# Optimization experiments

Hardware: AMD Instinct MI355X
Metric: run time of the kernel (lower is better)

Reference implementation:

```python
import jax, jax.numpy as jnp
import numpy as np

N = 24000; E = 384000; NT = 3; IN = 128; HID = 32; ED = 64; NE = 5; FFN = 64; C = 16
HEADS = (8, 8, 1); ALPHA = 0.05; DAL = 2


def _lrelu(x, s):
    return jnp.where(x >= 0, x, s * x)


def _elu(x):
    return jnp.where(x > 0, x, jnp.expm1(x))


def _ln(x, g, b, eps=1e-5):
    m = x.mean(-1, keepdims=True)
    v = ((x - m) ** 2).mean(-1, keepdims=True)
    return (x - m) / jnp.sqrt(v + eps) * g + b


def _l2n(x, eps=1e-12):
    return x / jnp.maximum(jnp.linalg.norm(x, axis=1, keepdims=True), eps)


def _ta(h, src, dst, e_feat, edge_emb, W, We, al, ar, ae, bias, res_W, res_attn, act):
    # SimpleHGN-style heterogeneous graph attention layer (TALayer)
    Hh = al.shape[0]
    feat = (h @ W).reshape(N, Hh, HID)                       # [N,H,D]
    ee = (edge_emb[e_feat] @ We).reshape(E, Hh, ED)          # [E,H,ED]
    el = (feat * al).sum(-1)                                 # [N,H]
    er = (feat * ar).sum(-1)                                 # [N,H]
    lg = _lrelu(el[src] + er[dst] + (ee * ae).sum(-1), 0.2)  # [E,H]
    m = jax.ops.segment_max(lg, dst, num_segments=N)         # edge softmax over dst
    a = jnp.exp(lg - m[dst])
    a = a / jax.ops.segment_sum(a, dst, num_segments=N)[dst]
    if res_attn is not None:
        a = a * (1.0 - ALPHA) + res_attn * ALPHA             # residual attention carry-over
    rst = jax.ops.segment_sum(a[:, :, None] * feat[src], dst, num_segments=N)
    if res_W is not None:
        rst = rst + (h @ res_W).reshape(N, Hh, HID)
    rst = rst + bias
    if act:
        rst = _elu(rst)
    return rst, jax.lax.stop_gradient(a)


def forward(feats, fc_W, fc_b, ntype_emb, W_ntype,
            ta0_edge_emb, ta0_W, ta0_We, ta0_al, ta0_ar, ta0_ae, ta0_bias,
            ta1_edge_emb, ta1_W, ta1_We, ta1_al, ta1_ar, ta1_ae, ta1_bias, ta1_res_W,
            ta2_edge_emb, ta2_W, ta2_We, ta2_al, ta2_ar, ta2_ae, ta2_bias, ta2_res_W,
            da_ln1_g, da_ln1_b, da_Wq, da_bq, da_Wk, da_bk, da_Wv, da_bv, da_Wo, da_bo,
            da_ln2_g, da_ln2_b, da_W1, da_b1, da_W2, da_b2, final_W, logits_W,
            e_feat, node_type, src, dst):
    # per-node-type input projection + leaky_relu(0.01), concat over types -> [N,HID]
    h = _lrelu(jnp.einsum('tni,tio->tno', feats, fc_W) + fc_b[:, None, :], 0.01).reshape(N, HID)
    ntype_feat = (ntype_emb @ W_ntype)[node_type]            # [N,HID]
    h = h * ntype_feat
    h0, a0 = _ta(h, src, dst, e_feat, ta0_edge_emb, ta0_W, ta0_We, ta0_al, ta0_ar, ta0_ae, ta0_bias, None, None, True)
    h = h0.reshape(N, -1)
    h1, _ = _ta(h, src, dst, e_feat, ta1_edge_emb, ta1_W, ta1_We, ta1_al, ta1_ar, ta1_ae, ta1_bias, ta1_res_W, a0, True)
    h = h1.reshape(N, -1)
    hf, _ = _ta(h, src, dst, e_feat, ta2_edge_emb, ta2_W, ta2_We, ta2_al, ta2_ar, ta2_ae, ta2_bias, ta2_res_W, None, False)
    h_feat = hf.reshape(N, HID)
    # dim-wise transformer (DALayer stack): tokens = HID dims, channel = 1
    x = (h_feat * ntype_feat)[:, :, None]                    # [N,HID,1]
    for l in range(DAL):
        y = _ln(x, da_ln1_g[l], da_ln1_b[l])
        q = y @ da_Wq[l] + da_bq[l]
        k = y @ da_Wk[l] + da_bk[l]
        v = y @ da_Wv[l] + da_bv[l]
        att = jax.nn.softmax(jnp.einsum('nqd,nkd->nqk', q, k), axis=-1)  # scale=att_size**-0.5=1
        x = x + (jnp.einsum('nqk,nkd->nqd', att, v) @ da_Wo[l] + da_bo[l])
        y = _ln(x, da_ln2_g[l], da_ln2_b[l])
        x = x + (jax.nn.gelu(y @ da_W1[l] + da_b1[l], approximate=False) @ da_W2[l] + da_b2[l])
    h_dim = _l2n(x[:, :, 0])
    h_final = jnp.concatenate([_l2n(h_feat), h_dim], axis=1) @ final_W
    logits = jax.nn.relu(h_final) @ logits_W
    return logits / jnp.maximum(jnp.linalg.norm(logits, axis=1, keepdims=True), 1e-12)


def setup_inputs():
    key = jax.random.key(0)
    ks = iter(jax.random.split(key, 96))
    def rn(shape, s=0.1):
        return jax.random.normal(next(ks), shape, jnp.float32) * s
    inp = {}
    inp["feats"] = jax.random.normal(next(ks), (NT, N // NT, IN), jnp.float32)
    inp["e_feat"] = jax.random.randint(next(ks), (E,), 0, NE)
    inp["node_type"] = jax.random.randint(next(ks), (N,), 0, NT)
    inp["src"] = jax.random.randint(next(ks), (E,), 0, N)
    inp["dst"] = jax.random.randint(next(ks), (E,), 0, N)
    inp["fc_W"] = rn((NT, IN, HID)); inp["fc_b"] = rn((NT, HID))
    inp["ntype_emb"] = rn((NT, HID)); inp["W_ntype"] = rn((HID, HID))
    ins = (HID, HID * HEADS[0], HID * HEADS[1])
    for l in range(3):
        Hh = HEADS[l]; di = ins[l]; p = "ta%d_" % l
        inp[p + "edge_emb"] = rn((NE, ED))
        inp[p + "W"] = rn((di, Hh * HID))
        inp[p + "We"] = rn((ED, Hh * ED))
        inp[p + "al"] = rn((Hh, HID)); inp[p + "ar"] = rn((Hh, HID)); inp[p + "ae"] = rn((Hh, ED))
        inp[p + "bias"] = jnp.zeros((Hh, HID), jnp.float32)
        if l > 0:
            inp[p + "res_W"] = rn((di, Hh * HID))
    inp["da_ln1_g"] = jnp.ones((DAL, 1), jnp.float32); inp["da_ln1_b"] = jnp.zeros((DAL, 1), jnp.float32)
    inp["da_Wq"] = rn((DAL, 1, 1)); inp["da_bq"] = jnp.zeros((DAL, 1), jnp.float32)
    inp["da_Wk"] = rn((DAL, 1, 1)); inp["da_bk"] = jnp.zeros((DAL, 1), jnp.float32)
    inp["da_Wv"] = rn((DAL, 1, 1)); inp["da_bv"] = jnp.zeros((DAL, 1), jnp.float32)
    inp["da_Wo"] = rn((DAL, 1, 1)); inp["da_bo"] = jnp.zeros((DAL, 1), jnp.float32)
    inp["da_ln2_g"] = jnp.ones((DAL, 1), jnp.float32); inp["da_ln2_b"] = jnp.zeros((DAL, 1), jnp.float32)
    inp["da_W1"] = rn((DAL, 1, FFN)); inp["da_b1"] = jnp.zeros((DAL, FFN), jnp.float32)
    inp["da_W2"] = rn((DAL, FFN, 1)); inp["da_b2"] = jnp.zeros((DAL, 1), jnp.float32)
    inp["final_W"] = rn((2 * HID, HID))
    inp["logits_W"] = rn((HID, C))
    return inp


def reference(feats, fc_W, fc_b, ntype_emb, W_ntype,
              ta0_edge_emb, ta0_W, ta0_We, ta0_al, ta0_ar, ta0_ae, ta0_bias,
              ta1_edge_emb, ta1_W, ta1_We, ta1_al, ta1_ar, ta1_ae, ta1_bias, ta1_res_W,
              ta2_edge_emb, ta2_W, ta2_We, ta2_al, ta2_ar, ta2_ae, ta2_bias, ta2_res_W,
              da_ln1_g, da_ln1_b, da_Wq, da_bq, da_Wk, da_bk, da_Wv, da_bv, da_Wo, da_bo,
              da_ln2_g, da_ln2_b, da_W1, da_b1, da_W2, da_b2, final_W, logits_W,
              e_feat, node_type, src, dst):
    return forward(feats, fc_W, fc_b, ntype_emb, W_ntype,
                   ta0_edge_emb, ta0_W, ta0_We, ta0_al, ta0_ar, ta0_ae, ta0_bias,
                   ta1_edge_emb, ta1_W, ta1_We, ta1_al, ta1_ar, ta1_ae, ta1_bias, ta1_res_W,
                   ta2_edge_emb, ta2_W, ta2_We, ta2_al, ta2_ar, ta2_ae, ta2_bias, ta2_res_W,
                   da_ln1_g, da_ln1_b, da_Wq, da_bq, da_Wk, da_bk, da_Wv, da_bv, da_Wo, da_bo,
                   da_ln2_g, da_ln2_b, da_W1, da_b1, da_W2, da_b2, final_W, logits_W,
                   e_feat, node_type, src, dst)
```

## Files before the change

### kernel.cpp

```cpp
#include <hip/hip_runtime.h>
#include <math.h>

constexpr int kN = 24000;
constexpr int kE = 384000;
constexpr float kAlpha = 0.05f;

typedef unsigned int   u32;
typedef unsigned short u16;
typedef __attribute__((ext_vector_type(8))) short short8;
typedef __attribute__((ext_vector_type(4))) float float4v;

__device__ __forceinline__ float bf2f(u16 x) { return __uint_as_float(((u32)x) << 16); }
__device__ __forceinline__ u16 f2bf(float f) {
  u32 u = __float_as_uint(f);
  return (u16)((u + 0x7fffu + ((u >> 16) & 1u)) >> 16);
}
__device__ __forceinline__ void bfrow32(const u16* __restrict__ p, float* f) {
  const uint4* q = (const uint4*)p;
  #pragma unroll
  for (int i = 0; i < 4; ++i) {
    uint4 w = q[i];
    f[i*8+0] = bf2f((u16)(w.x & 0xffff)); f[i*8+1] = bf2f((u16)(w.x >> 16));
    f[i*8+2] = bf2f((u16)(w.y & 0xffff)); f[i*8+3] = bf2f((u16)(w.y >> 16));
    f[i*8+4] = bf2f((u16)(w.z & 0xffff)); f[i*8+5] = bf2f((u16)(w.z >> 16));
    f[i*8+6] = bf2f((u16)(w.w & 0xffff)); f[i*8+7] = bf2f((u16)(w.w >> 16));
  }
}

__global__ void __launch_bounds__(256) zero_ints_kernel(int* __restrict__ p, int n) {
  int i = blockIdx.x * 256 + threadIdx.x;
  if (i < n) p[i] = 0;
}

__global__ void __launch_bounds__(256) count_kernel(const int* __restrict__ dst,
                                                    int* __restrict__ counts) {
  int e = blockIdx.x * 256 + threadIdx.x;
  if (e < kE) atomicAdd(&counts[dst[e]], 1);
}

__global__ void __launch_bounds__(1024) scan_kernel(const int* __restrict__ counts,
                                                    int* __restrict__ row_start) {
  __shared__ int wsum[16];
  __shared__ int carry_s;
  int tid = threadIdx.x, lane = tid & 63, wid = tid >> 6;
  if (tid == 0) { carry_s = 0; row_start[0] = 0; }
  __syncthreads();
  for (int base = 0; base < kN; base += 1024) {
    int x = (base + tid < kN) ? counts[base + tid] : 0;
    #pragma unroll
    for (int off = 1; off < 64; off <<= 1) {
      int y = __shfl_up(x, off);
      if (lane >= off) x += y;
    }
    if (lane == 63) wsum[wid] = x;
    __syncthreads();
    if (tid < 16) {
      int wv = wsum[tid];
      #pragma unroll
      for (int off = 1; off < 16; off <<= 1) {
        int y = __shfl_up(wv, off);
        if (tid >= off) wv += y;
      }
      wsum[tid] = wv;
    }
    __syncthreads();
    int incl = x + carry_s + (wid > 0 ? wsum[wid - 1] : 0);
    if (base + tid < kN) row_start[base + tid + 1] = incl;
    __syncthreads();
    if (tid == 1023) carry_s = incl;
    __syncthreads();
  }
}

__global__ void __launch_bounds__(256) scatter_kernel(const int* __restrict__ dst,
                                                      const int* __restrict__ row_start,
                                                      int* __restrict__ cursor,
                                                      int* __restrict__ edge_ids) {
  int e = blockIdx.x * 256 + threadIdx.x;
  if (e < kE) {
    int n = dst[e];
    int pos = row_start[n] + atomicAdd(&cursor[n], 1);
    edge_ids[pos] = e;
  }
}

__global__ void __launch_bounds__(256) prepack_kernel(
    const float* __restrict__ W0, const float* __restrict__ al0, const float* __restrict__ ar0,
    const float* __restrict__ W1, const float* __restrict__ al1, const float* __restrict__ ar1,
    const float* __restrict__ rW1,
    const float* __restrict__ W2, const float* __restrict__ al2, const float* __restrict__ ar2,
    const float* __restrict__ rW2,
    u16* __restrict__ WT0, u16* __restrict__ WT1, u16* __restrict__ WT2,
    const float* __restrict__ ntype_emb, const float* __restrict__ W_ntype,
    const float* __restrict__ emb0, const float* __restrict__ We0, const float* __restrict__ ae0,
    const float* __restrict__ emb1, const float* __restrict__ We1, const float* __restrict__ ae1,
    const float* __restrict__ emb2, const float* __restrict__ We2, const float* __restrict__ ae2,
    const float* __restrict__ ln1_b, const float* __restrict__ Wv, const float* __restrict__ bv,
    const float* __restrict__ Wo, const float* __restrict__ bo,
    const float* __restrict__ ln2_b, const float* __restrict__ DW1, const float* __restrict__ Db1,
    const float* __restrict__ DW2, const float* __restrict__ Db2,
    float* __restrict__ ntf, float* __restrict__ eterm, float* __restrict__ dadelta) {
  __shared__ float wae[17][64];
  __shared__ float red[128];
  int tid = threadIdx.x;
  if (blockIdx.x < 744) {
    const int SZ0 = 320 * 32, SZ1 = 576 * 256;
    int gid = blockIdx.x * 256 + tid;
    float v = 0.f;
    if (gid < SZ0) {
      int n = gid / 32, k = gid % 32;
      if (n < 256) v = W0[k * 256 + n];
      else if (n < 264) { int h = n - 256; for (int d = 0; d < 32; ++d) v += W0[k * 256 + h * 32 + d] * al0[h * 32 + d]; }
      else if (n < 272) { int h = n - 264; for (int d = 0; d < 32; ++d) v += W0[k * 256 + h * 32 + d] * ar0[h * 32 + d]; }
      WT0[n * 32 + k] = f2bf(v);
    } else if (gid < SZ0 + SZ1) {
      int i = gid - SZ0;
      int n = i / 256, k = i % 256;
      if (n < 256) v = W1[k * 256 + n];
      else if (n < 264) { int h = n - 256; for (int d = 0; d < 32; ++d) v += W1[k * 256 + h * 32 + d] * al1[h * 32 + d]; }
      else if (n < 272) { int h = n - 264; for (int d = 0; d < 32; ++d) v += W1[k * 256 + h * 32 + d] * ar1[h * 32 + d]; }
      else if (n < 528) v = rW1[k * 256 + (n - 272)];
      WT1[n * 256 + k] = f2bf(v);
    } else {
      int i = gid - SZ0 - SZ1;
      int n = i / 256, k = i % 256;
      if (n < 32) v = W2[k * 32 + n];
      else if (n == 32) { for (int d = 0; d < 32; ++d) v += W2[k * 32 + d] * al2[d]; }
      else if (n == 33) { for (int d = 0; d < 32; ++d) v += W2[k * 32 + d] * ar2[d]; }
      else if (n < 66) v = rW2[k * 32 + (n - 34)];
      WT2[n * 256 + k] = f2bf(v);
    }
  } else {
    for (int idx = tid; idx < 17 * 64; idx += 256) {
      int hg = idx >> 6, k = idx & 63;
      const float* We; const float* ae; int Hh, h;
      if (hg < 8)       { We = We0; ae = ae0; Hh = 8; h = hg; }
      else if (hg < 16) { We = We1; ae = ae1; Hh = 8; h = hg - 8; }
      else              { We = We2; ae = ae2; Hh = 1; h = 0; }
      float s = 0.f;
      for (int d = 0; d < 64; ++d) s += We[(size_t)k * Hh * 64 + h * 64 + d] * ae[h * 64 + d];
      wae[hg][k] = s;
    }
    __syncthreads();
    for (int id = tid; id < 85; id += 256) {
      const float* emb; int Hh, t, h, hg, base;
      if (id < 40)      { emb = emb0; Hh = 8; t = id / 8;  h = id % 8; hg = h;      base = 0;  }
      else if (id < 80) { int i = id - 40; emb = emb1; Hh = 8; t = i / 8; h = i % 8; hg = 8 + h; base = 40; }
      else              { int i = id - 80; emb = emb2; Hh = 1; t = i;    h = 0;     hg = 16;    base = 80; }
      float s = 0.f;
      for (int k = 0; k < 64; ++k) s += emb[t * 64 + k] * wae[hg][k];
      eterm[base + t * Hh + h] = s;
    }
    for (int idx = tid; idx < 96; idx += 256) {
      int t = idx / 32, o = idx % 32;
      float s = 0.f;
      for (int k = 0; k < 32; ++k) s += ntype_emb[t * 32 + k] * W_ntype[k * 32 + o];
      ntf[idx] = s;
    }
    for (int i2 = tid; i2 < 128; i2 += 256) {
      int l = i2 >> 6, j = i2 & 63;
      float u = ln2_b[l] * DW1[l * 64 + j] + Db1[l * 64 + j];
      float g = 0.5f * u * (1.0f + erff(u * 0.7071067811865476f));
      red[i2] = g * DW2[l * 64 + j];
    }
    __syncthreads();
    if (tid == 0) {
      float delta = 0.f;
      for (int l = 0; l < 2; ++l) {
        float vs = ln1_b[l] * Wv[l] + bv[l];
        delta += vs * Wo[l] + bo[l] + Db2[l];
      }
      for (int i = 0; i < 128; ++i) delta += red[i];
      *dadelta = delta;
    }
  }
}

__global__ void __launch_bounds__(256) inproj_kernel(
    const float* __restrict__ feats, const float* __restrict__ fc_W,
    const float* __restrict__ fc_b, const float* __restrict__ ntf,
    const int* __restrict__ node_type, u16* __restrict__ hb) {
  int t = blockIdx.x * 256 + threadIdx.x;
  if (t >= kN * 32) return;
  int n = t >> 5, o = t & 31;
  int ty = n / 8000;
  const float* fr = &feats[(size_t)n * 128];
  const float* w  = &fc_W[(size_t)ty * 4096 + o];
  float s = fc_b[ty * 32 + o];
  #pragma unroll
  for (int k = 0; k < 128; k += 4) {
    float4 f = *(const float4*)&fr[k];
    s += f.x * w[(k + 0) * 32] + f.y * w[(k + 1) * 32]
       + f.z * w[(k + 2) * 32] + f.w * w[(k + 3) * 32];
  }
  s = (s < 0.f) ? 0.01f * s : s;
  hb[t] = f2bf(s * ntf[node_type[n] * 32 + o]);
}

template <int K>
__global__ void __launch_bounds__(256) mfma_gemm_kernel(
    const u16* __restrict__ A, const u16* __restrict__ WT,
    const float* __restrict__ bias,
    u16* __restrict__ featb, float* __restrict__ el, float* __restrict__ er,
    u16* __restrict__ resb, float* __restrict__ resf,
    int N1, int HH, int N2) {
  constexpr int RB = K * 2;
  constexpr int CPR = K / 8;
  __shared__ __align__(16) u16 As[64 * K];
  __shared__ __align__(16) u16 Bs[64 * K];
  const int tid = threadIdx.x;
  const int l = tid & 63;
  const int w = tid >> 6;
  const int wm = w >> 1, wn = w & 1;
  const int m0 = blockIdx.y * 64;
  const int n0 = blockIdx.x * 64;
  const int kslot = l >> 4;
  const int l15 = l & 15;

  #pragma unroll
  for (int c = tid; c < 64 * CPR; c += 256) {
    int row = c / CPR, ch = c - row * CPR;
    int off = (row * RB + ch * 16) ^ ((row & 7) << 4);
    uint4 va = *(const uint4*)(A + (size_t)(m0 + row) * K + ch * 8);
    *(uint4*)((char*)As + off) = va;
    uint4 vb = *(const uint4*)(WT + (size_t)(n0 + row) * K + ch * 8);
    *(uint4*)((char*)Bs + off) = vb;
  }
  __syncthreads();

  float4v acc[2][2];
  #pragma unroll
  for (int f = 0; f < 2; ++f)
    #pragma unroll
    for (int g = 0; g < 2; ++g) { acc[f][g][0]=0.f; acc[f][g][1]=0.f; acc[f][g][2]=0.f; acc[f][g][3]=0.f; }

  #pragma unroll
  for (int kc = 0; kc < K; kc += 32) {
    short8 af[2], bf[2];
    #pragma unroll
    for (int f = 0; f < 2; ++f) {
      int row = wm * 32 + f * 16 + l15;
      int off = (row * RB + kc * 2 + kslot * 16) ^ ((row & 7) << 4);
      af[f] = *(const short8*)((const char*)As + off);
    }
    #pragma unroll
    for (int g = 0; g < 2; ++g) {
      int n = wn * 32 + g * 16 + l15;
      int off = (n * RB + kc * 2 + kslot * 16) ^ ((n & 7) << 4);
      bf[g] = *(const short8*)((const char*)Bs + off);
    }
    #pragma unroll
    for (int f = 0; f < 2; ++f)
      #pragma unroll
      for (int g = 0; g < 2; ++g)
        acc[f][g] = __builtin_amdgcn_mfma_f32_16x16x32_bf16(af[f], bf[g], acc[f][g], 0, 0, 0);
  }

  const int rbase = kslot * 4;
  #pragma unroll
  for (int f = 0; f < 2; ++f) {
    #pragma unroll
    for (int g = 0; g < 2; ++g) {
      int gc = n0 + wn * 32 + g * 16 + l15;
      #pragma unroll
      for (int reg = 0; reg < 4; ++reg) {
        int gr = m0 + wm * 32 + f * 16 + rbase + reg;
        float v = acc[f][g][reg];
        if (gc < N1) {
          featb[(size_t)gr * N1 + gc] = f2bf(v);
        } else if (gc < N1 + HH) {
          el[(size_t)gr * HH + (gc - N1)] = v;
        } else if (gc < N1 + 2 * HH) {
          er[(size_t)gr * HH + (gc - N1 - HH)] = v;
        } else if (gc < N1 + 2 * HH + N2) {
          int c2 = gc - N1 - 2 * HH;
          float vv = v + bias[c2];
          if (resb) resb[(size_t)gr * N2 + c2] = f2bf(vv);
          else      resf[(size_t)gr * N2 + c2] = vv;
        }
      }
    }
  }
}

template <bool WRITE_A0, bool READ_A0, bool BIAS_INIT, bool ACT>
__global__ void __launch_bounds__(256) agg8w_kernel(
    const int* __restrict__ row_start, const int* __restrict__ edge_ids,
    const int* __restrict__ src, const int* __restrict__ ef,
    const float* __restrict__ el, const float* __restrict__ er,
    const float* __restrict__ eterm,
    const u16* __restrict__ featb,
    const float* __restrict__ bias,
    _Float16* __restrict__ a0h,
    const u16* __restrict__ accb,
    u16* __restrict__ outb) {
  int n = (blockIdx.x * 256 + threadIdx.x) >> 6;
  if (n >= kN) return;
  int l = threadIdx.x & 63;
  int h = l >> 3, s = l & 7;
  int s0 = row_start[n], s1 = row_start[n + 1];
  float ern = er[n * 8 + h];
  float et0 = eterm[0 * 8 + h], et1 = eterm[1 * 8 + h], et2 = eterm[2 * 8 + h];
  float et3 = eterm[3 * 8 + h], et4 = eterm[4 * 8 + h];
  float m = -1e30f, ssum = 0.f;
  for (int i = s0 + s; i < s1; i += 8) {
    int e = edge_ids[i];
    int efc = ef[e];
    float etv = (efc == 0) ? et0 : (efc == 1) ? et1 : (efc == 2) ? et2 : (efc == 3) ? et3 : et4;
    float lg = el[src[e] * 8 + h] + ern + etv;
    lg = (lg < 0.f) ? 0.2f * lg : lg;
    if (lg > m) { ssum = ssum * expf(m - lg) + 1.f; m = lg; }
    else        { ssum += expf(lg - m); }
  }
  #pragma unroll
  for (int mk = 1; mk <= 4; mk <<= 1) {
    float om = __shfl_xor(m, mk);
    float os = __shfl_xor(ssum, mk);
    float nm = fmaxf(m, om);
    ssum = ssum * expf(m - nm) + os * expf(om - nm);
    m = nm;
  }
  float inv = 1.f / ssum;
  const size_t rowoff = (size_t)n * 256 + h * 32 + s * 4;
  float4 acc;
  if (BIAS_INIT) {
    acc = *(const float4*)(bias + h * 32 + s * 4);
  } else {
    ushort4 rv = *(const ushort4*)(accb + rowoff);
    acc = make_float4(bf2f(rv.x), bf2f(rv.y), bf2f(rv.z), bf2f(rv.w));
  }
  int i = s0;
  for (; i + 8 <= s1; i += 8) {
    int e = edge_ids[i + s];
    int sek = src[e];
    int efc = ef[e];
    float etv = (efc == 0) ? et0 : (efc == 1) ? et1 : (efc == 2) ? et2 : (efc == 3) ? et3 : et4;
    float lg = el[sek * 8 + h] + ern + etv;
    lg = (lg < 0.f) ? 0.2f * lg : lg;
    float am = expf(lg - m) * inv;
    if (WRITE_A0) a0h[(size_t)e * 8 + h] = (_Float16)am;
    if (READ_A0)  am = am * (1.f - kAlpha) + (float)a0h[(size_t)e * 8 + h] * kAlpha;
    #pragma unroll
    for (int j = 0; j < 8; ++j) {
      float aj = __shfl(am, (h << 3) + j);
      int sej = __shfl(sek, j);
      ushort4 fv = *(const ushort4*)(featb + (size_t)sej * 256 + h * 32 + s * 4);
      acc.x = fmaf(aj, bf2f(fv.x), acc.x);
      acc.y = fmaf(aj, bf2f(fv.y), acc.y);
      acc.z = fmaf(aj, bf2f(fv.z), acc.z);
      acc.w = fmaf(aj, bf2f(fv.w), acc.w);
    }
  }
  if (i < s1) {
    int cnt = s1 - i;
    float am = 0.f; int sek = 0;
    if (s < cnt) {
      int e = edge_ids[i + s];
      sek = src[e];
      int efc = ef[e];
      float etv = (efc == 0) ? et0 : (efc == 1) ? et1 : (efc == 2) ? et2 : (efc == 3) ? et3 : et4;
      float lg = el[sek * 8 + h] + ern + etv;
      lg = (lg < 0.f) ? 0.2f * lg : lg;
      am = expf(lg - m) * inv;
      if (WRITE_A0) a0h[(size_t)e * 8 + h] = (_Float16)am;
      if (READ_A0)  am = am * (1.f - kAlpha) + (float)a0h[(size_t)e * 8 + h] * kAlpha;
    }
    for (int j = 0; j < cnt; ++j) {
      float aj = __shfl(am, (h << 3) + j);
      int sej = __shfl(sek, j);
      ushort4 fv = *(const ushort4*)(featb + (size_t)sej * 256 + h * 32 + s * 4);
      acc.x = fmaf(aj, bf2f(fv.x), acc.x);
      acc.y = fmaf(aj, bf2f(fv.y), acc.y);
      acc.z = fmaf(aj, bf2f(fv.z), acc.z);
      acc.w = fmaf(aj, bf2f(fv.w), acc.w);
    }
  }
  if (ACT) {
    acc.x = (acc.x > 0.f) ? acc.x : expm1f(acc.x);
    acc.y = (acc.y > 0.f) ? acc.y : expm1f(acc.y);
    acc.z = (acc.z > 0.f) ? acc.z : expm1f(acc.z);
    acc.w = (acc.w > 0.f) ? acc.w : expm1f(acc.w);
  }
  ushort4 pw;
  pw.x = f2bf(acc.x); pw.y = f2bf(acc.y); pw.z = f2bf(acc.z); pw.w = f2bf(acc.w);
  *(ushort4*)(outb + rowoff) = pw;
}

__global__ void __launch_bounds__(256) agg1t_final_kernel(
    const int* __restrict__ row_start, const int* __restrict__ edge_ids,
    const int* __restrict__ src, const int* __restrict__ ef,
    const float* __restrict__ el, const float* __restrict__ er,
    const float* __restrict__ eterm,
    const u16* __restrict__ featb,
    const float* __restrict__ S2,
    const float* __restrict__ ntf, const int* __restrict__ node_type,
    const float* __restrict__ dadelta,
    const float* __restrict__ finalW, const float* __restrict__ logitsW,
    float* __restrict__ out) {
  int n = blockIdx.x * 256 + threadIdx.x;
  if (n >= kN) return;
  int s0 = row_start[n], s1 = row_start[n + 1];
  float ern = er[n];
  float et0 = eterm[0], et1 = eterm[1], et2 = eterm[2], et3 = eterm[3], et4 = eterm[4];
  float acc[32];
  #pragma unroll
  for (int d2 = 0; d2 < 8; ++d2) {
    float4 v = *(const float4*)&S2[(size_t)n * 32 + d2 * 4];
    acc[d2*4] = v.x; acc[d2*4+1] = v.y; acc[d2*4+2] = v.z; acc[d2*4+3] = v.w;
  }
  if (s0 < s1) {
    float m = -1e30f, ssum = 0.f;
    for (int i = s0; i < s1; ++i) {
      int e = edge_ids[i];
      int efc = ef[e];
      float etv = (efc == 0) ? et0 : (efc == 1) ? et1 : (efc == 2) ? et2 : (efc == 3) ? et3 : et4;
      float lg = el[src[e]] + ern + etv;
      lg = (lg < 0.f) ? 0.2f * lg : lg;
      if (lg > m) { ssum = ssum * expf(m - lg) + 1.f; m = lg; }
      else        { ssum += expf(lg - m); }
    }
    float inv = 1.f / ssum;
    int e0 = 0, se0 = 0, ef0 = 0;
    e0 = edge_ids[s0]; se0 = src[e0]; ef0 = ef[e0];
    for (int i = s0; i < s1; ++i) {
      int e = e0, se = se0, efc = ef0;
      if (i + 1 < s1) { e0 = edge_ids[i + 1]; se0 = src[e0]; ef0 = ef[e0]; }
      float etv = (efc == 0) ? et0 : (efc == 1) ? et1 : (efc == 2) ? et2 : (efc == 3) ? et3 : et4;
      float lg = el[se] + ern + etv;
      lg = (lg < 0.f) ? 0.2f * lg : lg;
      float a = expf(lg - m) * inv;
      float f[32];
      bfrow32(&featb[(size_t)se * 32], f);
      #pragma unroll
      for (int d = 0; d < 32; ++d) acc[d] = fmaf(a, f[d], acc[d]);
    }
  }
  float delta = dadelta[0];
  const float* nt = &ntf[node_type[n] * 32];
  float a_[32], b_[32];
  float na = 0.f, nb = 0.f;
  #pragma unroll
  for (int d = 0; d < 32; ++d) {
    float x = acc[d];
    a_[d] = x; na += x * x;
    float y = x * nt[d] + delta;
    b_[d] = y; nb += y * y;
  }
  float inva = 1.f / fmaxf(sqrtf(na), 1e-12f);
  float invb = 1.f / fmaxf(sqrtf(nb), 1e-12f);
  #pragma unroll
  for (int d = 0; d < 32; ++d) { a_[d] *= inva; b_[d] *= invb; }
  float lg[16];
  #pragma unroll
  for (int c = 0; c < 16; ++c) lg[c] = 0.f;
  for (int o = 0; o < 32; ++o) {
    float s = 0.f;
    #pragma unroll
    for (int d = 0; d < 32; ++d)
      s += a_[d] * finalW[d * 32 + o] + b_[d] * finalW[(32 + d) * 32 + o];
    s = fmaxf(s, 0.f);
    #pragma unroll
    for (int c = 0; c < 16; ++c) lg[c] += s * logitsW[o * 16 + c];
  }
  float nl = 0.f;
  #pragma unroll
  for (int c = 0; c < 16; ++c) nl += lg[c] * lg[c];
  float invl = 1.f / fmaxf(sqrtf(nl), 1e-12f);
  #pragma unroll
  for (int c = 0; c < 16; ++c) out[(size_t)n * 16 + c] = lg[c] * invl;
}

extern "C" void kernel_launch(void* const* d_in, const int* in_sizes, int n_in,
                              void* d_out, int out_size, void* d_ws, size_t ws_size,
                              hipStream_t stream) {
  const float* feats     = (const float*)d_in[0];
  const int*   e_feat    = (const int*)d_in[1];
  const int*   node_type = (const int*)d_in[2];
  const int*   src       = (const int*)d_in[3];
  const int*   dst       = (const int*)d_in[4];
  const float* fc_W      = (const float*)d_in[5];
  const float* fc_b      = (const float*)d_in[6];
  const float* ntype_emb = (const float*)d_in[7];
  const float* W_ntype   = (const float*)d_in[8];
  const float* ta_edge_emb[3] = {(const float*)d_in[9],  (const float*)d_in[16], (const float*)d_in[24]};
  const float* ta_W[3]        = {(const float*)d_in[10], (const float*)d_in[17], (const float*)d_in[25]};
  const float* ta_We[3]       = {(const float*)d_in[11], (const float*)d_in[18], (const float*)d_in[26]};
  const float* ta_al[3]       = {(const float*)d_in[12], (const float*)d_in[19], (const float*)d_in[27]};
  const float* ta_ar[3]       = {(const float*)d_in[13], (const float*)d_in[20], (const float*)d_in[28]};
  const float* ta_ae[3]       = {(const float*)d_in[14], (const float*)d_in[21], (const float*)d_in[29]};
  const float* ta_bias[3]     = {(const float*)d_in[15], (const float*)d_in[22], (const float*)d_in[30]};
  const float* ta1_res_W = (const float*)d_in[23];
  const float* ta2_res_W = (const float*)d_in[31];
  const float* da_ln1_b  = (const float*)d_in[33];
  const float* da_Wv     = (const float*)d_in[38];
  const float* da_bv     = (const float*)d_in[39];
  const float* da_Wo     = (const float*)d_in[40];
  const float* da_bo     = (const float*)d_in[41];
  const float* da_ln2_b  = (const float*)d_in[43];
  const float* da_W1     = (const float*)d_in[44];
  const float* da_b1     = (const float*)d_in[45];
  const float* da_W2     = (const float*)d_in[46];
  const float* da_b2     = (const float*)d_in[47];
  const float* final_W   = (const float*)d_in[48];
  const float* logits_W  = (const float*)d_in[49];
  float* out = (float*)d_out;

  char* base = (char*)d_ws;
  int* iws       = (int*)base;
  int* counts    = iws;
  int* cursor    = iws + kN;
  int* row_start = iws + 2 * kN;
  int* edge_ids  = iws + 2 * kN + kN + 1;
  char* p = base + (size_t)456004 * 4;
  float* ntf = (float*)p;                     p += 512;
  float* etm = (float*)p;                     p += 512;
  float* dad = (float*)p;                     p += 64;
  float* el  = (float*)p;                     p += (size_t)kN * 8 * 4;
  float* er  = (float*)p;                     p += (size_t)kN * 8 * 4;
  float* S2  = (float*)p;                     p += (size_t)kN * 32 * 4;
  u16*   Hb  = (u16*)p;                       p += (size_t)kN * 32 * 2;
  _Float16* a0h = (_Float16*)p;               p += (size_t)kE * 8 * 2;
  u16* featb = (u16*)p;                       p += (size_t)kN * 256 * 2;
  u16* Rb0   = (u16*)p;                       p += (size_t)kN * 256 * 2;
  u16* Rpr   = (u16*)p;                       p += (size_t)kN * 256 * 2;
  u16* WT0   = (u16*)p;                       p += (size_t)320 * 32 * 2;
  u16* WT1   = (u16*)p;                       p += (size_t)576 * 256 * 2;
  u16* WT2   = (u16*)p;                       p += (size_t)128 * 256 * 2;

  zero_ints_kernel<<<(2 * kN + 255) / 256, 256, 0, stream>>>(counts, 2 * kN);
  count_kernel<<<kE / 256, 256, 0, stream>>>(dst, counts);
  scan_kernel<<<1, 1024, 0, stream>>>(counts, row_start);
  scatter_kernel<<<kE / 256, 256, 0, stream>>>(dst, row_start, cursor, edge_ids);

  prepack_kernel<<<745, 256, 0, stream>>>(
      ta_W[0], ta_al[0], ta_ar[0],
      ta_W[1], ta_al[1], ta_ar[1], ta1_res_W,
      ta_W[2], ta_al[2], ta_ar[2], ta2_res_W,
      WT0, WT1, WT2,
      ntype_emb, W_ntype,
      ta_edge_emb[0], ta_We[0], ta_ae[0],
      ta_edge_emb[1], ta_We[1], ta_ae[1],
      ta_edge_emb[2], ta_We[2], ta_ae[2],
      da_ln1_b, da_Wv, da_bv, da_Wo, da_bo,
      da_ln2_b, da_W1, da_b1, da_W2, da_b2,
      ntf, etm, dad);

  inproj_kernel<<<(kN * 32) / 256, 256, 0, stream>>>(feats, fc_W, fc_b, ntf, node_type, Hb);

  mfma_gemm_kernel<32><<<dim3(5, kN / 64), 256, 0, stream>>>(
      Hb, WT0, nullptr, featb, el, er, nullptr, nullptr, 256, 8, 0);
  agg8w_kernel<true, false, true, true><<<kN / 4, 256, 0, stream>>>(
      row_start, edge_ids, src, e_feat, el, er, etm, featb, ta_bias[0], a0h, nullptr, Rb0);

  mfma_gemm_kernel<256><<<dim3(9, kN / 64), 256, 0, stream>>>(
      Rb0, WT1, ta_bias[1], featb, el, er, Rpr, nullptr, 256, 8, 256);
  agg8w_kernel<false, true, false, true><<<kN / 4, 256, 0, stream>>>(
      row_start, edge_ids, src, e_feat, el, er, etm + 40, featb, nullptr, a0h, Rpr, Rpr);

  mfma_gemm_kernel<256><<<dim3(2, kN / 64), 256, 0, stream>>>(
      Rpr, WT2, ta_bias[2], featb, el, er, nullptr, S2, 32, 1, 32);
  agg1t_final_kernel<<<(kN + 255) / 256, 256, 0, stream>>>(
      row_start, edge_ids, src, e_feat, el, er, etm + 80, featb, S2,
      ntf, node_type, dad, final_W, logits_W, out);
}
```

Measured before the change: 517.1 us.

## Use 32 lanes per node in final single-head aggregation and head kernel

Rewrites the last-layer aggregation plus final head so each node is processed by a 32-lane group instead of one thread. Lanes split the online softmax over edges and merge the partial max and sum with shuffles, then each lane owns one feature dimension and reads coalesced bf16 values. The final linear layers use weights staged in shared memory and per-node buffers with block barriers. The goal is to remove the old kernel's low parallelism (only 24000 threads), its heavy register use and its serial per-edge loop. The cost is more blocks, extra shuffles and more synchronization.

```diff
diff --git a/kernel.cpp b/kernel.cpp
--- a/kernel.cpp
+++ b/kernel.cpp
@@ -14,17 +14,6 @@
 __device__ __forceinline__ u16 f2bf(float f) {
   u32 u = __float_as_uint(f);
   return (u16)((u + 0x7fffu + ((u >> 16) & 1u)) >> 16);
-}
-__device__ __forceinline__ void bfrow32(const u16* __restrict__ p, float* f) {
-  const uint4* q = (const uint4*)p;
-  #pragma unroll
-  for (int i = 0; i < 4; ++i) {
-    uint4 w = q[i];
-    f[i*8+0] = bf2f((u16)(w.x & 0xffff)); f[i*8+1] = bf2f((u16)(w.x >> 16));
-    f[i*8+2] = bf2f((u16)(w.y & 0xffff)); f[i*8+3] = bf2f((u16)(w.y >> 16));
-    f[i*8+4] = bf2f((u16)(w.z & 0xffff)); f[i*8+5] = bf2f((u16)(w.z >> 16));
-    f[i*8+6] = bf2f((u16)(w.w & 0xffff)); f[i*8+7] = bf2f((u16)(w.w >> 16));
-  }
 }
 
 __global__ void __launch_bounds__(256) zero_ints_kernel(int* __restrict__ p, int n) {
@@ -386,7 +375,7 @@
   *(ushort4*)(outb + rowoff) = pw;
 }
 
-__global__ void __launch_bounds__(256) agg1t_final_kernel(
+__global__ void __launch_bounds__(256) aggw1_final_kernel(
     const int* __restrict__ row_start, const int* __restrict__ edge_ids,
     const int* __restrict__ src, const int* __restrict__ ef,
     const float* __restrict__ el, const float* __restrict__ er,
@@ -397,77 +386,108 @@
     const float* __restrict__ dadelta,
     const float* __restrict__ finalW, const float* __restrict__ logitsW,
     float* __restrict__ out) {
-  int n = blockIdx.x * 256 + threadIdx.x;
-  if (n >= kN) return;
-  int s0 = row_start[n], s1 = row_start[n + 1];
+  __shared__ float fWs[2048];
+  __shared__ float lWs[512];
+  __shared__ float abuf[8][32];
+  __shared__ float bbuf[8][32];
+  __shared__ float sbuf[8][32];
+  const int tid = threadIdx.x;
+  for (int i = tid; i < 2048; i += 256) fWs[i] = finalW[i];
+  for (int i = tid; i < 512; i += 256) lWs[i] = logitsW[i];
+  const int slot = tid >> 5;
+  const int g = tid & 31;
+  const int gb = tid & 32;
+  const int n = blockIdx.x * 8 + slot;
+  const int s0 = row_start[n], s1 = row_start[n + 1];
   float ern = er[n];
   float et0 = eterm[0], et1 = eterm[1], et2 = eterm[2], et3 = eterm[3], et4 = eterm[4];
-  float acc[32];
-  #pragma unroll
-  for (int d2 = 0; d2 < 8; ++d2) {
-    float4 v = *(const float4*)&S2[(size_t)n * 32 + d2 * 4];
-    acc[d2*4] = v.x; acc[d2*4+1] = v.y; acc[d2*4+2] = v.z; acc[d2*4+3] = v.w;
-  }
-  if (s0 < s1) {
-    float m = -1e30f, ssum = 0.f;
-    for (int i = s0; i < s1; ++i) {
-      int e = edge_ids[i];
+  float m = -1e30f, ssum = 0.f;
+  for (int i = s0 + g; i < s1; i += 32) {
+    int e = edge_ids[i];
+    int efc = ef[e];
+    float etv = (efc == 0) ? et0 : (efc == 1) ? et1 : (efc == 2) ? et2 : (efc == 3) ? et3 : et4;
+    float lg = el[src[e]] + ern + etv;
+    lg = (lg < 0.f) ? 0.2f * lg : lg;
+    if (lg > m) { ssum = ssum * expf(m - lg) + 1.f; m = lg; }
+    else        { ssum += expf(lg - m); }
+  }
+  #pragma unroll
+  for (int mk = 1; mk <= 16; mk <<= 1) {
+    float om = __shfl_xor(m, mk);
+    float os = __shfl_xor(ssum, mk);
+    float nm = fmaxf(m, om);
+    ssum = ssum * expf(m - nm) + os * expf(om - nm);
+    m = nm;
+  }
+  float inv = 1.f / ssum;
+  float acc = S2[(size_t)n * 32 + g];
+  int i = s0;
+  for (; i + 32 <= s1; i += 32) {
+    int e = edge_ids[i + g];
+    int sek = src[e];
+    int efc = ef[e];
+    float etv = (efc == 0) ? et0 : (efc == 1) ? et1 : (efc == 2) ? et2 : (efc == 3) ? et3 : et4;
+    float lg = el[sek] + ern + etv;
+    lg = (lg < 0.f) ? 0.2f * lg : lg;
+    float am = expf(lg - m) * inv;
+    #pragma unroll
+    for (int j = 0; j < 32; ++j) {
+      float aj = __shfl(am, gb + j);
+      int sej = __shfl(sek, gb + j);
+      acc = fmaf(aj, bf2f(featb[(size_t)sej * 32 + g]), acc);
+    }
+  }
+  if (i < s1) {
+    int cnt = s1 - i;
+    float am = 0.f; int sek = 0;
+    if (g < cnt) {
+      int e = edge_ids[i + g];
+      sek = src[e];
       int efc = ef[e];
       float etv = (efc == 0) ? et0 : (efc == 1) ? et1 : (efc == 2) ? et2 : (efc == 3) ? et3 : et4;
-      float lg = el[src[e]] + ern + etv;
+      float lg = el[sek] + ern + etv;
       lg = (lg < 0.f) ? 0.2f * lg : lg;
-      if (lg > m) { ssum = ssum * expf(m - lg) + 1.f; m = lg; }
-      else        { ssum += expf(lg - m); }
-    }
-    float inv = 1.f / ssum;
-    int e0 = 0, se0 = 0, ef0 = 0;
-    e0 = edge_ids[s0]; se0 = src[e0]; ef0 = ef[e0];
-    for (int i = s0; i < s1; ++i) {
-      int e = e0, se = se0, efc = ef0;
-      if (i + 1 < s1) { e0 = edge_ids[i + 1]; se0 = src[e0]; ef0 = ef[e0]; }
-      float etv = (efc == 0) ? et0 : (efc == 1) ? et1 : (efc == 2) ? et2 : (efc == 3) ? et3 : et4;
-      float lg = el[se] + ern + etv;
-      lg = (lg < 0.f) ? 0.2f * lg : lg;
-      float a = expf(lg - m) * inv;
-      float f[32];
-      bfrow32(&featb[(size_t)se * 32], f);
-      #pragma unroll
-      for (int d = 0; d < 32; ++d) acc[d] = fmaf(a, f[d], acc[d]);
+      am = expf(lg - m) * inv;
+    }
+    for (int j = 0; j < cnt; ++j) {
+      float aj = __shfl(am, gb + j);
+      int sej = __shfl(sek, gb + j);
+      acc = fmaf(aj, bf2f(featb[(size_t)sej * 32 + g]), acc);
     }
   }
   float delta = dadelta[0];
-  const float* nt = &ntf[node_type[n] * 32];
-  float a_[32], b_[32];
-  float na = 0.f, nb = 0.f;
-  #pragma unroll
-  for (int d = 0; d < 32; ++d) {
-    float x = acc[d];
-    a_[d] = x; na += x * x;
-    float y = x * nt[d] + delta;
-    b_[d] = y; nb += y * y;
+  float ntv = ntf[node_type[n] * 32 + g];
+  float av = acc;
+  float bv = acc * ntv + delta;
+  float na = av * av, nb = bv * bv;
+  #pragma unroll
+  for (int mk = 1; mk <= 16; mk <<= 1) {
+    na += __shfl_xor(na, mk);
+    nb += __shfl_xor(nb, mk);
   }
   float inva = 1.f / fmaxf(sqrtf(na), 1e-12f);
   float invb = 1.f / fmaxf(sqrtf(nb), 1e-12f);
-  #pragma unroll
-  for (int d = 0; d < 32; ++d) { a_[d] *= inva; b_[d] *= invb; }
-  float lg[16];
-  #pragma unroll
-  for (int c = 0; c < 16; ++c) lg[c] = 0.f;
-  for (int o = 0; o < 32; ++o) {
-    float s = 0.f;
-    #pragma unroll
-    for (int d = 0; d < 32; ++d)
-      s += a_[d] * finalW[d * 32 + o] + b_[d] * finalW[(32 + d) * 32 + o];
-    s = fmaxf(s, 0.f);
-    #pragma unroll
-    for (int c = 0; c < 16; ++c) lg[c] += s * logitsW[o * 16 + c];
-  }
-  float nl = 0.f;
-  #pragma unroll
-  for (int c = 0; c < 16; ++c) nl += lg[c] * lg[c];
-  float invl = 1.f / fmaxf(sqrtf(nl), 1e-12f);
-  #pragma unroll
-  for (int c = 0; c < 16; ++c) out[(size_t)n * 16 + c] = lg[c] * invl;
+  __syncthreads();
+  abuf[slot][g] = av * inva;
+  bbuf[slot][g] = bv * invb;
+  __syncthreads();
+  float s = 0.f;
+  #pragma unroll
+  for (int d = 0; d < 32; ++d)
+    s += abuf[slot][d] * fWs[d * 32 + g] + bbuf[slot][d] * fWs[(32 + d) * 32 + g];
+  s = fmaxf(s, 0.f);
+  sbuf[slot][g] = s;
+  __syncthreads();
+  if (g < 16) {
+    float lg = 0.f;
+    #pragma unroll
+    for (int o = 0; o < 32; ++o) lg += sbuf[slot][o] * lWs[o * 16 + g];
+    float nl = lg * lg;
+    #pragma unroll
+    for (int mk = 1; mk <= 8; mk <<= 1) nl += __shfl_xor(nl, mk);
+    float invl = 1.f / fmaxf(sqrtf(nl), 1e-12f);
+    out[(size_t)n * 16 + g] = lg * invl;
+  }
 }
 
 extern "C" void kernel_launch(void* const* d_in, const int* in_sizes, int n_in,
@@ -559,7 +579,7 @@
 
   mfma_gemm_kernel<256><<<dim3(2, kN / 64), 256, 0, stream>>>(
       Rpr, WT2, ta_bias[2], featb, el, er, nullptr, S2, 32, 1, 32);
-  agg1t_final_kernel<<<(kN + 255) / 256, 256, 0, stream>>>(
+  aggw1_final_kernel<<<kN / 8, 256, 0, stream>>>(
       row_start, edge_ids, src, e_feat, el, er, etm + 80, featb, S2,
       ntf, node_type, dad, final_W, logits_W, out);
 }
```

Measured after the change: 487.2 us. -5.8%, faster.
